# Kernel optimization log

Hardware: AMD Instinct MI355X
Metric: run time of the kernel (lower is better)

## Reference

```python
import jax, jax.numpy as jnp
import numpy as np

EPS = 1e-05
QN, QP = -128.0, 127.0


def setup_inputs() -> dict:
    key = jax.random.key(0)
    kx, kw = jax.random.split(key)
    x = jax.random.normal(kx, (4, 2048, 4096), dtype=jnp.float32)
    weight = jax.random.normal(kw, (4096, 4096), dtype=jnp.float32)  # [out, in]
    return {"x": x, "weight": weight}


def reference(x, weight):
    # --- per-token int8 activation quantization (activation_quant) ---
    # s: [B, S, 1], scale so that max(|x|) maps to 127
    s = QP / jnp.clip(jnp.max(jnp.abs(x), axis=-1, keepdims=True), 1e-05, None)
    q = jnp.clip(jnp.round(x * s), QN, QP)  # int8-valued, kept in float
    xq = q / s  # dequantized activations fed to the matmul

    # --- ternary weight quantization (terniarize + pack/unpack round-trip) ---
    scale_w = 1.0 / jnp.clip(jnp.mean(jnp.abs(weight)), EPS, None)
    tw = jnp.clip(jnp.round(weight * scale_w), -1.0, 1.0)  # ternary {-1,0,1}, [out, in]

    # --- bitmat: (xq) @ tw^T, then dequant by weight scale ---
    out = jnp.einsum('bsi,oi->bso', xq, tw) / scale_w
    return out
```

## Files before the change

### kernel.cpp

```cpp
#include <hip/hip_runtime.h>
#include <stdint.h>

#define K_DIM 4096
#define M_TOK 8192
#define N_OUT 4096

typedef int v4i __attribute__((ext_vector_type(4)));
typedef int v16i __attribute__((ext_vector_type(16)));


#define BAR()                                     \
    do {                                          \
        asm volatile("" ::: "memory");            \
        __builtin_amdgcn_s_barrier();             \
        asm volatile("" ::: "memory");            \
    } while (0)

__device__ __forceinline__ void gload_lds16(const void* g, void* l) {
    auto gp = reinterpret_cast<const __attribute__((address_space(1))) uint32_t*>(
        reinterpret_cast<uintptr_t>(g));
    auto lp = reinterpret_cast<__attribute__((address_space(3))) uint32_t*>(
        reinterpret_cast<uintptr_t>(l));
    __builtin_amdgcn_global_load_lds(gp, lp, 16, 0, 0);
}

__global__ __launch_bounds__(256) void quant_act(const float* __restrict__ x,
                                                 int8_t* __restrict__ q,
                                                 float* __restrict__ rs,
                                                 double* __restrict__ acc) {
    const int token = blockIdx.x;
    const int t = threadIdx.x;
    if (token == 0 && t == 0) *acc = 0.0;
    const float4* x4 = (const float4*)(x + (size_t)token * K_DIM);
    float4 v[4];
    float m = 0.0f;
#pragma unroll
    for (int r = 0; r < 4; ++r) {
        v[r] = x4[t + 256 * r];
        m = fmaxf(m, fmaxf(fmaxf(fabsf(v[r].x), fabsf(v[r].y)),
                           fmaxf(fabsf(v[r].z), fabsf(v[r].w))));
    }
#pragma unroll
    for (int off = 32; off; off >>= 1) m = fmaxf(m, __shfl_down(m, off, 64));
    __shared__ float wmax[4];
    __shared__ float smax;
    if ((t & 63) == 0) wmax[t >> 6] = m;
    __syncthreads();
    if (t == 0) smax = fmaxf(fmaxf(wmax[0], wmax[1]), fmaxf(wmax[2], wmax[3]));
    __syncthreads();
    const float s = 127.0f / fmaxf(smax, 1e-5f);
    char4* q4 = (char4*)(q + (size_t)token * K_DIM);
#pragma unroll
    for (int r = 0; r < 4; ++r) {
        float4 f = v[r];
        char4 c;
        c.x = (signed char)fminf(fmaxf(rintf(f.x * s), -128.0f), 127.0f);
        c.y = (signed char)fminf(fmaxf(rintf(f.y * s), -128.0f), 127.0f);
        c.z = (signed char)fminf(fmaxf(rintf(f.z * s), -128.0f), 127.0f);
        c.w = (signed char)fminf(fmaxf(rintf(f.w * s), -128.0f), 127.0f);
        q4[t + 256 * r] = c;
    }
    if (t == 0) rs[token] = 1.0f / s;
}

__global__ __launch_bounds__(256) void wabs_sum(const float* __restrict__ w,
                                                double* __restrict__ acc) {
    const size_t n4 = (size_t)N_OUT * K_DIM / 4;
    const size_t stride = (size_t)gridDim.x * 256;
    const float4* w4 = (const float4*)w;
    float sum = 0.0f;
    for (size_t j = (size_t)blockIdx.x * 256 + threadIdx.x; j < n4; j += stride) {
        float4 f = w4[j];
        sum += fabsf(f.x) + fabsf(f.y) + fabsf(f.z) + fabsf(f.w);
    }
    double d = (double)sum;
#pragma unroll
    for (int off = 32; off; off >>= 1) d += __shfl_down(d, off, 64);
    __shared__ double wsum[4];
    const int t = threadIdx.x;
    if ((t & 63) == 0) wsum[t >> 6] = d;
    __syncthreads();
    if (t == 0) atomicAdd(acc, wsum[0] + wsum[1] + wsum[2] + wsum[3]);
}

__global__ __launch_bounds__(256) void ternarize(const float* __restrict__ w,
                                                 int8_t* __restrict__ tw,
                                                 const double* __restrict__ acc) {
    const double mean = *acc * (1.0 / ((double)N_OUT * (double)K_DIM));
    const float sw = 1.0f / fmaxf((float)mean, 1e-5f);
    const size_t i = (size_t)blockIdx.x * 256 + threadIdx.x;
    const float4* w4 = (const float4*)w;
    char4* t4 = (char4*)tw;
    float4 f = w4[i];
    char4 c;
    c.x = (signed char)fminf(fmaxf(rintf(f.x * sw), -1.0f), 1.0f);
    c.y = (signed char)fminf(fmaxf(rintf(f.y * sw), -1.0f), 1.0f);
    c.z = (signed char)fminf(fmaxf(rintf(f.z * sw), -1.0f), 1.0f);
    c.w = (signed char)fminf(fmaxf(rintf(f.w * sw), -1.0f), 1.0f);
    t4[i] = c;
}

__global__ __launch_bounds__(512, 2) void gemm_i8(const int8_t* __restrict__ A,
                                                  const int8_t* __restrict__ B,
                                                  const float* __restrict__ rs,
                                                  const double* __restrict__ acc,
                                                  float* __restrict__ out) {
    const int nwgx = N_OUT / 256;
    const int orig = blockIdx.y * nwgx + blockIdx.x;
    const int wg = (orig & 7) * 64 + (orig >> 3);
    const int bm = (wg / nwgx) * 256;
    const int bn = (wg % nwgx) * 256;

    __shared__ int8_t smem[4][2][16384];

    const int t0 = threadIdx.x;
    const int lane = t0 & 63;
    const int wave = t0 >> 6;
    const int wm = (wave >> 1) * 64;
    const int wn = (wave & 1) * 128;

    v16i accv[2][4] = {};

    const int R0 = t0 >> 2;
    const int scol = (((t0 & 3) ^ (R0 & 3) ^ ((R0 >> 2) & 3)) << 4);
    const int8_t* Ag = A + (size_t)(bm + R0) * K_DIM + scol;
    const int8_t* Bg = B + (size_t)(bn + R0) * K_DIM + scol;
    int8_t* ldst = &smem[0][0][0] + (size_t)t0 * 16;

    const int l31 = lane & 31;
    const int lh = lane >> 5;
    const int sx = (l31 & 3) ^ ((l31 >> 2) & 3);

#pragma unroll
    for (int pt = 0; pt < 3; ++pt) {
        const int k0 = pt * 64;
        int8_t* sb = ldst + pt * 32768;
        gload_lds16(Ag + k0, sb);
        gload_lds16(Ag + k0 + (size_t)128 * K_DIM, sb + 8192);
        gload_lds16(Bg + k0, sb + 16384);
        gload_lds16(Bg + k0 + (size_t)128 * K_DIM, sb + 24576);
    }
    asm volatile("s_waitcnt vmcnt(8)" ::: "memory");
    BAR();

#pragma unroll 1
    for (int t = 0; t < 64; ++t) {
        const int slot = t & 3;
        const int8_t* aB = &smem[slot][0][0];
        const int8_t* bB = &smem[slot][1][0];
        const bool st = (t < 61);
        const int ksg = (t + 3) * 64;
        int8_t* sb = ldst + ((t + 3) & 3) * 32768;

#pragma unroll
        for (int ks = 0; ks < 2; ++ks) {
            const int co = (((ks * 2 + lh) ^ sx) << 4);
            v4i af0 = *(const v4i*)(aB + (wm + l31) * 64 + co);
            v4i af1 = *(const v4i*)(aB + (wm + 32 + l31) * 64 + co);
            v4i bf[4];
#pragma unroll
            for (int n = 0; n < 4; ++n)
                bf[n] = *(const v4i*)(bB + (wn + n * 32 + l31) * 64 + co);
            if (st) {
                if (ks == 0) {
                    gload_lds16(Ag + ksg, sb);
                    gload_lds16(Ag + ksg + (size_t)128 * K_DIM, sb + 8192);
                } else {
                    gload_lds16(Bg + ksg, sb + 16384);
                    gload_lds16(Bg + ksg + (size_t)128 * K_DIM, sb + 24576);
                }
            }
            BAR();
            __builtin_amdgcn_s_setprio(1);
#pragma unroll
            for (int n = 0; n < 4; ++n) {
                accv[0][n] = __builtin_amdgcn_mfma_i32_32x32x32_i8(af0, bf[n], accv[0][n], 0, 0, 0);
                accv[1][n] = __builtin_amdgcn_mfma_i32_32x32x32_i8(af1, bf[n], accv[1][n], 0, 0, 0);
            }
            __builtin_amdgcn_s_setprio(0);
            if (ks == 0) BAR();
        }
        if (t < 61) asm volatile("s_waitcnt vmcnt(8)" ::: "memory");
        else if (t == 61) asm volatile("s_waitcnt vmcnt(4)" ::: "memory");
        else if (t == 62) asm volatile("s_waitcnt vmcnt(0)" ::: "memory");
        if (t < 63) BAR();
    }

    const double mean = *acc * (1.0 / ((double)N_OUT * (double)K_DIM));
    const float wmean = fmaxf((float)mean, 1e-5f);
#pragma unroll
    for (int m = 0; m < 2; ++m) {
#pragma unroll
        for (int r = 0; r < 16; ++r) {
            const int row = bm + wm + m * 32 + (r & 3) + 8 * (r >> 2) + 4 * lh;
            const float scale = rs[row] * wmean;
            float* orow = out + (size_t)row * N_OUT + bn + wn + l31;
#pragma unroll
            for (int n = 0; n < 4; ++n)
                orow[n * 32] = (float)accv[m][n][r] * scale;
        }
    }
}

extern "C" void kernel_launch(void* const* d_in, const int* in_sizes, int n_in,
                              void* d_out, int out_size, void* d_ws, size_t ws_size,
                              hipStream_t stream) {
    const float* x = (const float*)d_in[0];
    const float* w = (const float*)d_in[1];
    float* out = (float*)d_out;
    char* ws = (char*)d_ws;
    int8_t* q = (int8_t*)ws;
    int8_t* tw = (int8_t*)(ws + 33554432);
    float* rs = (float*)(ws + 50331648);
    double* acc = (double*)(ws + 50364416);

    hipLaunchKernelGGL(quant_act, dim3(M_TOK), dim3(256), 0, stream, x, q, rs, acc);
    hipLaunchKernelGGL(wabs_sum, dim3(1024), dim3(256), 0, stream, w, acc);
    hipLaunchKernelGGL(ternarize, dim3((N_OUT * (size_t)K_DIM / 4) / 256), dim3(256), 0, stream, w, tw, acc);
    hipLaunchKernelGGL(gemm_i8, dim3(N_OUT / 256, M_TOK / 256), dim3(512), 0, stream, q, tw, rs, acc, out);
}
```

Baseline: 410.6 us.

## Software-pipeline LDS fragment loads in int8 GEMM and replace atomic weight-sum reduction

The GEMM main loop now prefetches the next K-step's first-half LDS fragments while issuing MFMAs on the current ones, and drops the mid-iteration barrier. This gives one barrier per iteration instead of two and overlaps LDS reads with matrix math. All four global-to-LDS loads are issued at the top of each iteration. The weight abs-sum now writes per-block partials instead of using a double atomicAdd, and ternarize reduces those partials itself while processing four float4s per thread. Each ternarize block redundantly re-reduces the 1024 partials, and the fragment prefetch raises register pressure.

```diff
diff --git a/kernel.cpp b/kernel.cpp
--- a/kernel.cpp
+++ b/kernel.cpp
@@ -26,11 +26,9 @@
 
 __global__ __launch_bounds__(256) void quant_act(const float* __restrict__ x,
                                                  int8_t* __restrict__ q,
-                                                 float* __restrict__ rs,
-                                                 double* __restrict__ acc) {
+                                                 float* __restrict__ rs) {
     const int token = blockIdx.x;
     const int t = threadIdx.x;
-    if (token == 0 && t == 0) *acc = 0.0;
     const float4* x4 = (const float4*)(x + (size_t)token * K_DIM);
     float4 v[4];
     float m = 0.0f;
@@ -64,7 +62,7 @@
 }
 
 __global__ __launch_bounds__(256) void wabs_sum(const float* __restrict__ w,
-                                                double* __restrict__ acc) {
+                                                double* __restrict__ partial) {
     const size_t n4 = (size_t)N_OUT * K_DIM / 4;
     const size_t stride = (size_t)gridDim.x * 256;
     const float4* w4 = (const float4*)w;
@@ -80,30 +78,43 @@
     const int t = threadIdx.x;
     if ((t & 63) == 0) wsum[t >> 6] = d;
     __syncthreads();
-    if (t == 0) atomicAdd(acc, wsum[0] + wsum[1] + wsum[2] + wsum[3]);
+    if (t == 0) partial[blockIdx.x] = wsum[0] + wsum[1] + wsum[2] + wsum[3];
 }
 
 __global__ __launch_bounds__(256) void ternarize(const float* __restrict__ w,
                                                  int8_t* __restrict__ tw,
-                                                 const double* __restrict__ acc) {
-    const double mean = *acc * (1.0 / ((double)N_OUT * (double)K_DIM));
-    const float sw = 1.0f / fmaxf((float)mean, 1e-5f);
-    const size_t i = (size_t)blockIdx.x * 256 + threadIdx.x;
+                                                 const double* __restrict__ partial,
+                                                 float* __restrict__ meanp) {
+    const int t = threadIdx.x;
+    double d = partial[t] + partial[t + 256] + partial[t + 512] + partial[t + 768];
+#pragma unroll
+    for (int off = 32; off; off >>= 1) d += __shfl_down(d, off, 64);
+    __shared__ double pr[4];
+    if ((t & 63) == 0) pr[t >> 6] = d;
+    __syncthreads();
+    const double tot = pr[0] + pr[1] + pr[2] + pr[3];
+    const float mean = fmaxf((float)(tot * (1.0 / ((double)N_OUT * (double)K_DIM))), 1e-5f);
+    const float sw = 1.0f / mean;
+    if (blockIdx.x == 0 && t == 0) *meanp = mean;
     const float4* w4 = (const float4*)w;
     char4* t4 = (char4*)tw;
-    float4 f = w4[i];
-    char4 c;
-    c.x = (signed char)fminf(fmaxf(rintf(f.x * sw), -1.0f), 1.0f);
-    c.y = (signed char)fminf(fmaxf(rintf(f.y * sw), -1.0f), 1.0f);
-    c.z = (signed char)fminf(fmaxf(rintf(f.z * sw), -1.0f), 1.0f);
-    c.w = (signed char)fminf(fmaxf(rintf(f.w * sw), -1.0f), 1.0f);
-    t4[i] = c;
+    const size_t base = (size_t)blockIdx.x * 1024 + t;
+#pragma unroll
+    for (int r = 0; r < 4; ++r) {
+        float4 f = w4[base + r * 256];
+        char4 c;
+        c.x = (signed char)fminf(fmaxf(rintf(f.x * sw), -1.0f), 1.0f);
+        c.y = (signed char)fminf(fmaxf(rintf(f.y * sw), -1.0f), 1.0f);
+        c.z = (signed char)fminf(fmaxf(rintf(f.z * sw), -1.0f), 1.0f);
+        c.w = (signed char)fminf(fmaxf(rintf(f.w * sw), -1.0f), 1.0f);
+        t4[base + r * 256] = c;
+    }
 }
 
 __global__ __launch_bounds__(512, 2) void gemm_i8(const int8_t* __restrict__ A,
                                                   const int8_t* __restrict__ B,
                                                   const float* __restrict__ rs,
-                                                  const double* __restrict__ acc,
+                                                  const float* __restrict__ meanp,
                                                   float* __restrict__ out) {
     const int nwgx = N_OUT / 256;
     const int orig = blockIdx.y * nwgx + blockIdx.x;
@@ -130,6 +141,14 @@
     const int l31 = lane & 31;
     const int lh = lane >> 5;
     const int sx = (l31 & 3) ^ ((l31 >> 2) & 3);
+    const int co0 = ((lh ^ sx) << 4);
+    const int co1 = (((2 + lh) ^ sx) << 4);
+    const int offA0 = (wm + l31) * 64;
+    const int offA1 = (wm + 32 + l31) * 64;
+    const int offB0 = (wn + l31) * 64;
+    const int offB1 = (wn + 32 + l31) * 64;
+    const int offB2 = (wn + 64 + l31) * 64;
+    const int offB3 = (wn + 96 + l31) * 64;
 
 #pragma unroll
     for (int pt = 0; pt < 3; ++pt) {
@@ -143,51 +162,80 @@
     asm volatile("s_waitcnt vmcnt(8)" ::: "memory");
     BAR();
 
+    v4i ca0, ca1, cb0, cb1, cb2, cb3;
+    {
+        const int8_t* aB = &smem[0][0][0];
+        const int8_t* bB = &smem[0][1][0];
+        ca0 = *(const v4i*)(aB + offA0 + co0);
+        ca1 = *(const v4i*)(aB + offA1 + co0);
+        cb0 = *(const v4i*)(bB + offB0 + co0);
+        cb1 = *(const v4i*)(bB + offB1 + co0);
+        cb2 = *(const v4i*)(bB + offB2 + co0);
+        cb3 = *(const v4i*)(bB + offB3 + co0);
+    }
+
 #pragma unroll 1
     for (int t = 0; t < 64; ++t) {
         const int slot = t & 3;
         const int8_t* aB = &smem[slot][0][0];
         const int8_t* bB = &smem[slot][1][0];
-        const bool st = (t < 61);
-        const int ksg = (t + 3) * 64;
-        int8_t* sb = ldst + ((t + 3) & 3) * 32768;
-
-#pragma unroll
-        for (int ks = 0; ks < 2; ++ks) {
-            const int co = (((ks * 2 + lh) ^ sx) << 4);
-            v4i af0 = *(const v4i*)(aB + (wm + l31) * 64 + co);
-            v4i af1 = *(const v4i*)(aB + (wm + 32 + l31) * 64 + co);
-            v4i bf[4];
-#pragma unroll
-            for (int n = 0; n < 4; ++n)
-                bf[n] = *(const v4i*)(bB + (wn + n * 32 + l31) * 64 + co);
-            if (st) {
-                if (ks == 0) {
-                    gload_lds16(Ag + ksg, sb);
-                    gload_lds16(Ag + ksg + (size_t)128 * K_DIM, sb + 8192);
-                } else {
-                    gload_lds16(Bg + ksg, sb + 16384);
-                    gload_lds16(Bg + ksg + (size_t)128 * K_DIM, sb + 24576);
-                }
-            }
-            BAR();
-            __builtin_amdgcn_s_setprio(1);
-#pragma unroll
-            for (int n = 0; n < 4; ++n) {
-                accv[0][n] = __builtin_amdgcn_mfma_i32_32x32x32_i8(af0, bf[n], accv[0][n], 0, 0, 0);
-                accv[1][n] = __builtin_amdgcn_mfma_i32_32x32x32_i8(af1, bf[n], accv[1][n], 0, 0, 0);
-            }
-            __builtin_amdgcn_s_setprio(0);
-            if (ks == 0) BAR();
+
+        if (t < 61) {
+            const int ksg = (t + 3) * 64;
+            int8_t* sb = ldst + ((t + 3) & 3) * 32768;
+            gload_lds16(Ag + ksg, sb);
+            gload_lds16(Ag + ksg + (size_t)128 * K_DIM, sb + 8192);
+            gload_lds16(Bg + ksg, sb + 16384);
+            gload_lds16(Bg + ksg + (size_t)128 * K_DIM, sb + 24576);
         }
+
+        v4i na0 = *(const v4i*)(aB + offA0 + co1);
+        v4i na1 = *(const v4i*)(aB + offA1 + co1);
+        v4i nb0 = *(const v4i*)(bB + offB0 + co1);
+        v4i nb1 = *(const v4i*)(bB + offB1 + co1);
+        v4i nb2 = *(const v4i*)(bB + offB2 + co1);
+        v4i nb3 = *(const v4i*)(bB + offB3 + co1);
+
+        __builtin_amdgcn_s_setprio(1);
+        accv[0][0] = __builtin_amdgcn_mfma_i32_32x32x32_i8(ca0, cb0, accv[0][0], 0, 0, 0);
+        accv[1][0] = __builtin_amdgcn_mfma_i32_32x32x32_i8(ca1, cb0, accv[1][0], 0, 0, 0);
+        accv[0][1] = __builtin_amdgcn_mfma_i32_32x32x32_i8(ca0, cb1, accv[0][1], 0, 0, 0);
+        accv[1][1] = __builtin_amdgcn_mfma_i32_32x32x32_i8(ca1, cb1, accv[1][1], 0, 0, 0);
+        accv[0][2] = __builtin_amdgcn_mfma_i32_32x32x32_i8(ca0, cb2, accv[0][2], 0, 0, 0);
+        accv[1][2] = __builtin_amdgcn_mfma_i32_32x32x32_i8(ca1, cb2, accv[1][2], 0, 0, 0);
+        accv[0][3] = __builtin_amdgcn_mfma_i32_32x32x32_i8(ca0, cb3, accv[0][3], 0, 0, 0);
+        accv[1][3] = __builtin_amdgcn_mfma_i32_32x32x32_i8(ca1, cb3, accv[1][3], 0, 0, 0);
+        __builtin_amdgcn_s_setprio(0);
+
         if (t < 61) asm volatile("s_waitcnt vmcnt(8)" ::: "memory");
         else if (t == 61) asm volatile("s_waitcnt vmcnt(4)" ::: "memory");
         else if (t == 62) asm volatile("s_waitcnt vmcnt(0)" ::: "memory");
-        if (t < 63) BAR();
-    }
-
-    const double mean = *acc * (1.0 / ((double)N_OUT * (double)K_DIM));
-    const float wmean = fmaxf((float)mean, 1e-5f);
+        if (t < 63) {
+            BAR();
+            const int nslot = (t + 1) & 3;
+            const int8_t* aN = &smem[nslot][0][0];
+            const int8_t* bN = &smem[nslot][1][0];
+            ca0 = *(const v4i*)(aN + offA0 + co0);
+            ca1 = *(const v4i*)(aN + offA1 + co0);
+            cb0 = *(const v4i*)(bN + offB0 + co0);
+            cb1 = *(const v4i*)(bN + offB1 + co0);
+            cb2 = *(const v4i*)(bN + offB2 + co0);
+            cb3 = *(const v4i*)(bN + offB3 + co0);
+        }
+
+        __builtin_amdgcn_s_setprio(1);
+        accv[0][0] = __builtin_amdgcn_mfma_i32_32x32x32_i8(na0, nb0, accv[0][0], 0, 0, 0);
+        accv[1][0] = __builtin_amdgcn_mfma_i32_32x32x32_i8(na1, nb0, accv[1][0], 0, 0, 0);
+        accv[0][1] = __builtin_amdgcn_mfma_i32_32x32x32_i8(na0, nb1, accv[0][1], 0, 0, 0);
+        accv[1][1] = __builtin_amdgcn_mfma_i32_32x32x32_i8(na1, nb1, accv[1][1], 0, 0, 0);
+        accv[0][2] = __builtin_amdgcn_mfma_i32_32x32x32_i8(na0, nb2, accv[0][2], 0, 0, 0);
+        accv[1][2] = __builtin_amdgcn_mfma_i32_32x32x32_i8(na1, nb2, accv[1][2], 0, 0, 0);
+        accv[0][3] = __builtin_amdgcn_mfma_i32_32x32x32_i8(na0, nb3, accv[0][3], 0, 0, 0);
+        accv[1][3] = __builtin_amdgcn_mfma_i32_32x32x32_i8(na1, nb3, accv[1][3], 0, 0, 0);
+        __builtin_amdgcn_s_setprio(0);
+    }
+
+    const float wmean = *meanp;
 #pragma unroll
     for (int m = 0; m < 2; ++m) {
 #pragma unroll
@@ -212,10 +260,11 @@
     int8_t* q = (int8_t*)ws;
     int8_t* tw = (int8_t*)(ws + 33554432);
     float* rs = (float*)(ws + 50331648);
-    double* acc = (double*)(ws + 50364416);
-
-    hipLaunchKernelGGL(quant_act, dim3(M_TOK), dim3(256), 0, stream, x, q, rs, acc);
-    hipLaunchKernelGGL(wabs_sum, dim3(1024), dim3(256), 0, stream, w, acc);
-    hipLaunchKernelGGL(ternarize, dim3((N_OUT * (size_t)K_DIM / 4) / 256), dim3(256), 0, stream, w, tw, acc);
-    hipLaunchKernelGGL(gemm_i8, dim3(N_OUT / 256, M_TOK / 256), dim3(512), 0, stream, q, tw, rs, acc, out);
-}
+    double* partial = (double*)(ws + 50364416);
+    float* meanp = (float*)(ws + 50372608);
+
+    hipLaunchKernelGGL(quant_act, dim3(M_TOK), dim3(256), 0, stream, x, q, rs);
+    hipLaunchKernelGGL(wabs_sum, dim3(1024), dim3(256), 0, stream, w, partial);
+    hipLaunchKernelGGL(ternarize, dim3((N_OUT * (size_t)K_DIM / 16) / 256), dim3(256), 0, stream, w, tw, partial, meanp);
+    hipLaunchKernelGGL(gemm_i8, dim3(N_OUT / 256, M_TOK / 256), dim3(512), 0, stream, q, tw, rs, meanp, out);
+}
```

After: 405.1 us. No clear change (-1.3%).
